# Performance work log

Measured on AMD Instinct MI355X. Metric: run time of the kernel, lower is better.

## Reference

```python
import jax, jax.numpy as jnp
import numpy as np

B, N, C, K, OUT = 4, 10000, 128, 16, 128


def setup_inputs() -> dict:
    key = jax.random.key(0)
    k1, k2, k3, k4 = jax.random.split(key, 4)
    x = jax.random.normal(k1, (B, N, C), dtype=jnp.float32)
    edge_index = jax.random.randint(k2, (2, B, N, K), 0, N)
    # Linear(2C -> OUT), torch convention W: [OUT, 2C]
    W = jax.random.normal(k3, (OUT, 2 * C), dtype=jnp.float32) * 0.05
    b = jax.random.normal(k4, (OUT,), dtype=jnp.float32) * 0.05
    return {"x": x, "edge_index": edge_index, "W": W, "b": b}


def reference(x, edge_index, W, b):
    # x: [B, N, C] -> [B, C, N]
    xt = jnp.swapaxes(x, 1, 2)
    Bs, Cs, Ns = xt.shape
    # batched_index_select: [C, N] gathered by [N, K] -> [C, N, K], vmapped over batch
    gather = jax.vmap(lambda xb, ib: xb[:, ib])
    x_i = gather(xt, edge_index[1])  # [B, C, N, K]
    x_j = gather(xt, edge_index[0])  # [B, C, N, K]
    rel = jnp.max(x_j - x_i, axis=-1)  # max-relative: [B, C, N]
    # interleave channels: [x_0, rel_0, x_1, rel_1, ...] -> [B, 2C, N]
    feat = jnp.stack([xt, rel], axis=2).reshape(Bs, 2 * Cs, Ns)
    feat = jnp.swapaxes(feat, 1, 2)  # [B, N, 2C]
    out = feat @ W.T + b  # Linear(2C -> OUT)
    return jax.nn.relu(out)
```

## Files before the change

### kernel.cpp

```cpp
#include <hip/hip_runtime.h>


#define Bn 4
#define Nn 10000
#define Cn 128
#define Kn 16
#define OUTn 128
#define Mn 16
#define FPAD 8

typedef _Float16 half8v __attribute__((ext_vector_type(8)));
typedef float floatx4 __attribute__((ext_vector_type(4)));

__global__ __launch_bounds__(256) void prep(const float* __restrict__ x,
                                            const float* __restrict__ W,
                                            _Float16* __restrict__ xh,
                                            _Float16* __restrict__ Wh) {
    if (blockIdx.x < 2500) {
        int i = blockIdx.x * 256 + threadIdx.x;
        const float4* x4 = (const float4*)x;
        float4 a = x4[2 * i];
        float4 c = x4[2 * i + 1];
        union { _Float16 h[8]; uint4 q; } pk;
        pk.h[0] = (_Float16)a.x; pk.h[1] = (_Float16)a.y;
        pk.h[2] = (_Float16)a.z; pk.h[3] = (_Float16)a.w;
        pk.h[4] = (_Float16)c.x; pk.h[5] = (_Float16)c.y;
        pk.h[6] = (_Float16)c.z; pk.h[7] = (_Float16)c.w;
        *(uint4*)(xh + 8 * (size_t)i) = pk.q;
    } else {
        int tid = (blockIdx.x - 2500) * 256 + threadIdx.x;
        int lane = tid & 63;
        int step = (tid >> 6) & 7;
        int tile = tid >> 9;
        int o = tile * 16 + (lane & 15);
        int quad = lane >> 4;
        union { _Float16 h[8]; uint4 q; } pk;
#pragma unroll
        for (int j = 0; j < 8; ++j) {
            int c2 = step * 32 + quad * 8 + j;
            pk.h[j] = (_Float16)W[o * (2 * Cn) + c2];
        }
        *(uint4*)(Wh + (size_t)tid * 8) = pk.q;
    }
}

__global__ __launch_bounds__(256, 4) void mrconv_kernel(
    const _Float16* __restrict__ xh, const int* __restrict__ edge,
    const _Float16* __restrict__ Wh, const float* __restrict__ bias,
    float* __restrict__ out)
{
    __shared__ _Float16 sfeat[Mn][2 * Cn + FPAD];
    __shared__ int sidx[2][Mn][Kn];

    int bi = blockIdx.x;
    int slot = bi & 7;
    int b = slot & 3;
    int nb = (bi >> 3) * 2 + (slot >> 2);
    if (nb >= Nn / Mn) return;
    const int n0 = nb * Mn;
    const int gbase = b * Nn + n0;

    const int t = threadIdx.x;
    const int wv = t >> 6;
    const int lane = t & 63;

    for (int i = t; i < 2 * Mn * Kn; i += 256) {
        int s = i >> 8;
        int m = (i >> 4) & 15;
        int k = i & 15;
        sidx[s][m][k] = edge[s * (Bn * Nn * Kn) + (gbase + m) * Kn + k];
    }
    __syncthreads();

    const _Float16* xbb = xh + (size_t)b * Nn * Cn;

    {
        const int q = lane >> 4;
        const int l16 = lane & 15;
        const int m = wv * 4 + q;
        const int ch = l16 * 8;
        const half8v xs = *(const half8v*)(xbb + (n0 + m) * Cn + ch);
        half8v r;
#pragma unroll
        for (int e = 0; e < 8; ++e) r[e] = (_Float16)(-65504.0f);
#pragma unroll
        for (int kc = 0; kc < 2; ++kc) {
            half8v vj[8], vi[8];
#pragma unroll
            for (int u = 0; u < 8; ++u) {
                const int jj = sidx[0][m][kc * 8 + u];
                const int ii = sidx[1][m][kc * 8 + u];
                vj[u] = *(const half8v*)(xbb + jj * Cn + ch);
                vi[u] = *(const half8v*)(xbb + ii * Cn + ch);
            }
#pragma unroll
            for (int u = 0; u < 8; ++u) {
                half8v d = vj[u] - vi[u];
                r = __builtin_elementwise_max(r, d);
            }
        }
        union { _Float16 h[16]; uint4 q[2]; } pk;
#pragma unroll
        for (int e = 0; e < 8; ++e) {
            pk.h[2 * e] = xs[e];
            pk.h[2 * e + 1] = r[e];
        }
        *(uint4*)&sfeat[m][2 * ch] = pk.q[0];
        *(uint4*)&sfeat[m][2 * ch + 8] = pk.q[1];
    }
    __syncthreads();

    const int m16 = lane & 15;
    const int quad = lane >> 4;
    floatx4 acc0 = {0.f, 0.f, 0.f, 0.f};
    floatx4 acc1 = {0.f, 0.f, 0.f, 0.f};
    const half8v* wh8 = (const half8v*)Wh;
    const int tile0 = 2 * wv, tile1 = 2 * wv + 1;
#pragma unroll
    for (int step = 0; step < 8; ++step) {
        half8v a = *(const half8v*)&sfeat[m16][step * 32 + quad * 8];
        half8v b0 = wh8[(tile0 * 8 + step) * 64 + lane];
        half8v b1 = wh8[(tile1 * 8 + step) * 64 + lane];
        acc0 = __builtin_amdgcn_mfma_f32_16x16x32_f16(a, b0, acc0, 0, 0, 0);
        acc1 = __builtin_amdgcn_mfma_f32_16x16x32_f16(a, b1, acc1, 0, 0, 0);
    }
    const int o0 = tile0 * 16 + m16;
    const int o1 = tile1 * 16 + m16;
    const float bb0 = bias[o0], bb1 = bias[o1];
#pragma unroll
    for (int r = 0; r < 4; ++r) {
        int g = gbase + quad * 4 + r;
        out[g * OUTn + o0] = fmaxf(acc0[r] + bb0, 0.f);
        out[g * OUTn + o1] = fmaxf(acc1[r] + bb1, 0.f);
    }
}

extern "C" void kernel_launch(void* const* d_in, const int* in_sizes, int n_in,
                              void* d_out, int out_size, void* d_ws, size_t ws_size,
                              hipStream_t stream) {
    const float* x = (const float*)d_in[0];
    const int* edge = (const int*)d_in[1];
    const float* W = (const float*)d_in[2];
    const float* bias = (const float*)d_in[3];
    float* out = (float*)d_out;

    _Float16* Wh = (_Float16*)d_ws;
    _Float16* xh = (_Float16*)((char*)d_ws + 65536);

    prep<<<2516, 256, 0, stream>>>(x, W, xh, Wh);
    mrconv_kernel<<<2560, 256, 0, stream>>>(xh, edge, Wh, bias, out);
}
```

Measured before the change: 102.7 us.

## Double threads per block, split neighbor gather across lanes with shuffle reduction

The main kernel now runs 512 threads per block instead of 256. Each node's 16 neighbors are split between two lane groups, each taking alternating k, and the two partial maxima are combined with a cross-lane xor-16 shuffle. The GEMM stage gives each of the 8 waves one output tile instead of two. The aim is more memory-level parallelism per node in the latency-bound gather, with fewer registers per thread, at the cost of an extra shuffle, half the lanes idle during the shared-memory store, and a different launch grid.

```diff
diff --git a/kernel.cpp b/kernel.cpp
--- a/kernel.cpp
+++ b/kernel.cpp
@@ -44,7 +44,7 @@
     }
 }
 
-__global__ __launch_bounds__(256, 4) void mrconv_kernel(
+__global__ __launch_bounds__(512, 8) void mrconv_kernel(
     const _Float16* __restrict__ xh, const int* __restrict__ edge,
     const _Float16* __restrict__ Wh, const float* __restrict__ bias,
     float* __restrict__ out)
@@ -64,10 +64,10 @@
     const int wv = t >> 6;
     const int lane = t & 63;
 
-    for (int i = t; i < 2 * Mn * Kn; i += 256) {
-        int s = i >> 8;
-        int m = (i >> 4) & 15;
-        int k = i & 15;
+    {
+        int s = t >> 8;
+        int m = (t >> 4) & 15;
+        int k = t & 15;
         sidx[s][m][k] = edge[s * (Bn * Nn * Kn) + (gbase + m) * Kn + k];
     }
     __syncthreads();
@@ -77,61 +77,66 @@
     {
         const int q = lane >> 4;
         const int l16 = lane & 15;
-        const int m = wv * 4 + q;
+        const int nd = q >> 1;
+        const int m = 2 * wv + nd;
+        const int kq = q & 1;
         const int ch = l16 * 8;
         const half8v xs = *(const half8v*)(xbb + (n0 + m) * Cn + ch);
         half8v r;
 #pragma unroll
         for (int e = 0; e < 8; ++e) r[e] = (_Float16)(-65504.0f);
 #pragma unroll
-        for (int kc = 0; kc < 2; ++kc) {
-            half8v vj[8], vi[8];
+        for (int cc = 0; cc < 2; ++cc) {
+            half8v vj[4], vi[4];
 #pragma unroll
-            for (int u = 0; u < 8; ++u) {
-                const int jj = sidx[0][m][kc * 8 + u];
-                const int ii = sidx[1][m][kc * 8 + u];
+            for (int u = 0; u < 4; ++u) {
+                const int k = 2 * (cc * 4 + u) + kq;
+                const int jj = sidx[0][m][k];
+                const int ii = sidx[1][m][k];
                 vj[u] = *(const half8v*)(xbb + jj * Cn + ch);
                 vi[u] = *(const half8v*)(xbb + ii * Cn + ch);
             }
 #pragma unroll
-            for (int u = 0; u < 8; ++u) {
+            for (int u = 0; u < 4; ++u) {
                 half8v d = vj[u] - vi[u];
                 r = __builtin_elementwise_max(r, d);
             }
         }
-        union { _Float16 h[16]; uint4 q[2]; } pk;
+        union { half8v h; unsigned u[4]; } rr, rs;
+        rr.h = r;
 #pragma unroll
-        for (int e = 0; e < 8; ++e) {
-            pk.h[2 * e] = xs[e];
-            pk.h[2 * e + 1] = r[e];
+        for (int e = 0; e < 4; ++e)
+            rs.u[e] = (unsigned)__shfl_xor((int)rr.u[e], 16, 64);
+        rr.h = __builtin_elementwise_max(rr.h, rs.h);
+        if (kq == 0) {
+            union { _Float16 h[16]; uint4 qq[2]; } pk;
+#pragma unroll
+            for (int e = 0; e < 8; ++e) {
+                pk.h[2 * e] = xs[e];
+                pk.h[2 * e + 1] = rr.h[e];
+            }
+            *(uint4*)&sfeat[m][2 * ch] = pk.qq[0];
+            *(uint4*)&sfeat[m][2 * ch + 8] = pk.qq[1];
         }
-        *(uint4*)&sfeat[m][2 * ch] = pk.q[0];
-        *(uint4*)&sfeat[m][2 * ch + 8] = pk.q[1];
     }
     __syncthreads();
 
     const int m16 = lane & 15;
     const int quad = lane >> 4;
-    floatx4 acc0 = {0.f, 0.f, 0.f, 0.f};
-    floatx4 acc1 = {0.f, 0.f, 0.f, 0.f};
+    floatx4 acc = {0.f, 0.f, 0.f, 0.f};
     const half8v* wh8 = (const half8v*)Wh;
-    const int tile0 = 2 * wv, tile1 = 2 * wv + 1;
 #pragma unroll
     for (int step = 0; step < 8; ++step) {
         half8v a = *(const half8v*)&sfeat[m16][step * 32 + quad * 8];
-        half8v b0 = wh8[(tile0 * 8 + step) * 64 + lane];
-        half8v b1 = wh8[(tile1 * 8 + step) * 64 + lane];
-        acc0 = __builtin_amdgcn_mfma_f32_16x16x32_f16(a, b0, acc0, 0, 0, 0);
-        acc1 = __builtin_amdgcn_mfma_f32_16x16x32_f16(a, b1, acc1, 0, 0, 0);
+        half8v bf = wh8[(wv * 8 + step) * 64 + lane];
+        acc = __builtin_amdgcn_mfma_f32_16x16x32_f16(a, bf, acc, 0, 0, 0);
     }
-    const int o0 = tile0 * 16 + m16;
-    const int o1 = tile1 * 16 + m16;
-    const float bb0 = bias[o0], bb1 = bias[o1];
+    const int o = wv * 16 + m16;
+    const float bb = bias[o];
 #pragma unroll
-    for (int r = 0; r < 4; ++r) {
-        int g = gbase + quad * 4 + r;
-        out[g * OUTn + o0] = fmaxf(acc0[r] + bb0, 0.f);
-        out[g * OUTn + o1] = fmaxf(acc1[r] + bb1, 0.f);
+    for (int rI = 0; rI < 4; ++rI) {
+        int g = gbase + quad * 4 + rI;
+        out[g * OUTn + o] = fmaxf(acc[rI] + bb, 0.f);
     }
 }
 
@@ -148,5 +153,5 @@
     _Float16* xh = (_Float16*)((char*)d_ws + 65536);
 
     prep<<<2516, 256, 0, stream>>>(x, W, xh, Wh);
-    mrconv_kernel<<<2560, 256, 0, stream>>>(xh, edge, Wh, bias, out);
+    mrconv_kernel<<<2504, 512, 0, stream>>>(xh, edge, Wh, bias, out);
 }
```

Result: slower. 133.1 us (+29.5%).
